# Kernel tuning notes

Measured on AMD Instinct MI355X. Metric: run time of the kernel, lower is better.

## Reference

```python
import jax, jax.numpy as jnp
import numpy as np

D = 3  # feature dim fixed by the module's Linear(3,3) layers
N = 6144

def _linear(x, w, b):
    # torch Linear: y = x @ W^T + b, W: [out,in]
    return x @ w.T + b

def setup_inputs() -> dict:
    key = jax.random.key(0)
    ks = jax.random.split(key, 20)
    lim = 1.0 / np.sqrt(D)  # torch default init bound
    def W(k):
        return jax.random.uniform(k, (D, D), jnp.float32, -lim, lim)
    def B(k):
        return jax.random.uniform(k, (D,), jnp.float32, -lim, lim)
    inp = {"x_data": jax.random.normal(ks[0], (N, D), jnp.float32)}
    names = ["q1", "q2", "q3", "q4", "k1", "k2", "v1", "v2", "b1b2"]
    for i, nm in enumerate(names):
        inp["w_" + nm] = W(ks[1 + 2 * i])
        inp["b_" + nm] = B(ks[2 + 2 * i])
    return inp

def reference(x_data, w_q1, b_q1, w_q2, b_q2, w_q3, b_q3, w_q4, b_q4,
              w_k1, b_k1, w_k2, b_k2, w_v1, b_v1, w_v2, b_v2, w_b1b2, b_b1b2):
    k1 = _linear(x_data, w_k1, b_k1)
    k2 = _linear(x_data, w_k2, b_k2)
    group1 = _linear(x_data, w_q1, b_q1) + _linear(x_data, w_q2, b_q2)
    group2 = _linear(x_data, w_q3, b_q3) + _linear(x_data, w_q4, b_q4)
    a1 = jax.nn.softmax(group1 @ k1.T, axis=1)  # [N, N]
    a2 = jax.nn.softmax(group2 @ k2.T, axis=1)  # [N, N]
    v1 = _linear(x_data, w_v1, b_v1)
    v2 = _linear(x_data, w_v2, b_v2)
    b = _linear(a1 @ v1 + a2 @ v2, w_b1b2, b_b1b2)  # [N, D]
    return (a1, b)
```

## Files before the change

kernel.cpp:

```cpp
#include <hip/hip_runtime.h>
#include <cstddef>

#define N_ROWS 6144
#define TR 8
#define NT 256
#define NBLK (N_ROWS / TR)

__device__ __forceinline__ float wredMax(float v) {
#pragma unroll
    for (int off = 32; off > 0; off >>= 1) v = fmaxf(v, __shfl_xor(v, off, 64));
    return v;
}
__device__ __forceinline__ float wredSum(float v) {
#pragma unroll
    for (int off = 32; off > 0; off >>= 1) v += __shfl_xor(v, off, 64);
    return v;
}

__global__ void proj_kernel(
    const float* __restrict__ x,
    const float* __restrict__ wq1, const float* __restrict__ bq1,
    const float* __restrict__ wq2, const float* __restrict__ bq2,
    const float* __restrict__ wq3, const float* __restrict__ bq3,
    const float* __restrict__ wq4, const float* __restrict__ bq4,
    const float* __restrict__ wk1, const float* __restrict__ bk1,
    const float* __restrict__ wk2, const float* __restrict__ bk2,
    const float* __restrict__ wv1, const float* __restrict__ bv1,
    const float* __restrict__ wv2, const float* __restrict__ bv2,
    float* __restrict__ gpack, float* __restrict__ kpack, float* __restrict__ vpack)
{
    int i = blockIdx.x * blockDim.x + threadIdx.x;
    if (i >= N_ROWS) return;
    float x0 = x[3*i+0], x1 = x[3*i+1], x2 = x[3*i+2];

    float g[8], k[8], v[8];
#pragma unroll
    for (int o = 0; o < 3; o++) {
        g[o]   = (wq1[3*o+0]+wq2[3*o+0])*x0 + (wq1[3*o+1]+wq2[3*o+1])*x1
               + (wq1[3*o+2]+wq2[3*o+2])*x2 + bq1[o] + bq2[o];
        g[3+o] = (wq3[3*o+0]+wq4[3*o+0])*x0 + (wq3[3*o+1]+wq4[3*o+1])*x1
               + (wq3[3*o+2]+wq4[3*o+2])*x2 + bq3[o] + bq4[o];
        k[o]   = wk1[3*o+0]*x0 + wk1[3*o+1]*x1 + wk1[3*o+2]*x2 + bk1[o];
        k[3+o] = wk2[3*o+0]*x0 + wk2[3*o+1]*x1 + wk2[3*o+2]*x2 + bk2[o];
        v[o]   = wv1[3*o+0]*x0 + wv1[3*o+1]*x1 + wv1[3*o+2]*x2 + bv1[o];
        v[3+o] = wv2[3*o+0]*x0 + wv2[3*o+1]*x1 + wv2[3*o+2]*x2 + bv2[o];
    }
    g[6]=g[7]=k[6]=k[7]=v[6]=v[7]=0.f;

    *(float4*)(gpack + (size_t)i*8)     = make_float4(g[0],g[1],g[2],g[3]);
    *(float4*)(gpack + (size_t)i*8 + 4) = make_float4(g[4],g[5],g[6],g[7]);
    *(float4*)(kpack + (size_t)i*8)     = make_float4(k[0],k[1],k[2],k[3]);
    *(float4*)(kpack + (size_t)i*8 + 4) = make_float4(k[4],k[5],k[6],k[7]);
    *(float4*)(vpack + (size_t)i*8)     = make_float4(v[0],v[1],v[2],v[3]);
    *(float4*)(vpack + (size_t)i*8 + 4) = make_float4(v[4],v[5],v[6],v[7]);
}

__global__ __launch_bounds__(NT) void attn_kernel(
    const float* __restrict__ gpack, const float* __restrict__ kpack,
    const float* __restrict__ vpack,
    const float* __restrict__ wb, const float* __restrict__ bb,
    float* __restrict__ out)
{
    const int row0 = blockIdx.x * TR;
    const int tid  = threadIdx.x;
    const int wave = tid >> 6;
    const int lane = tid & 63;

    __shared__ float red[4][3*TR];

    float g1x[TR], g1y[TR], g1z[TR], g2x[TR], g2y[TR], g2z[TR];
#pragma unroll
    for (int r = 0; r < TR; r++) {
        const float* gp = gpack + (size_t)(row0 + r) * 8;
        g1x[r]=gp[0]; g1y[r]=gp[1]; g1z[r]=gp[2];
        g2x[r]=gp[3]; g2y[r]=gp[4]; g2z[r]=gp[5];
    }

    float m1[TR], m2[TR];
#pragma unroll
    for (int r = 0; r < TR; r++) { m1[r] = -1e30f; m2[r] = -1e30f; }

    for (int j = tid; j < N_ROWS; j += NT) {
        const float4 ka = *(const float4*)(kpack + (size_t)j*8);
        const float2 kb = *(const float2*)(kpack + (size_t)j*8 + 4);
#pragma unroll
        for (int r = 0; r < TR; r++) {
            float s1 = g1x[r]*ka.x + g1y[r]*ka.y + g1z[r]*ka.z;
            float s2 = g2x[r]*ka.w + g2y[r]*kb.x + g2z[r]*kb.y;
            m1[r] = fmaxf(m1[r], s1);
            m2[r] = fmaxf(m2[r], s2);
        }
    }
#pragma unroll
    for (int r = 0; r < TR; r++) { m1[r] = wredMax(m1[r]); m2[r] = wredMax(m2[r]); }
    if (lane == 0) {
#pragma unroll
        for (int r = 0; r < TR; r++) { red[wave][r] = m1[r]; red[wave][TR+r] = m2[r]; }
    }
    __syncthreads();
#pragma unroll
    for (int r = 0; r < TR; r++) {
        m1[r] = fmaxf(fmaxf(red[0][r],    red[1][r]),    fmaxf(red[2][r],    red[3][r]));
        m2[r] = fmaxf(fmaxf(red[0][TR+r], red[1][TR+r]), fmaxf(red[2][TR+r], red[3][TR+r]));
    }
    __syncthreads();

    float l1[TR], l2[TR];
#pragma unroll
    for (int r = 0; r < TR; r++) { l1[r] = 0.f; l2[r] = 0.f; }

    for (int j = tid; j < N_ROWS; j += NT) {
        const float4 ka = *(const float4*)(kpack + (size_t)j*8);
        const float2 kb = *(const float2*)(kpack + (size_t)j*8 + 4);
#pragma unroll
        for (int r = 0; r < TR; r++) {
            float s1 = g1x[r]*ka.x + g1y[r]*ka.y + g1z[r]*ka.z;
            float s2 = g2x[r]*ka.w + g2y[r]*kb.x + g2z[r]*kb.y;
            l1[r] += __expf(s1 - m1[r]);
            l2[r] += __expf(s2 - m2[r]);
        }
    }
#pragma unroll
    for (int r = 0; r < TR; r++) { l1[r] = wredSum(l1[r]); l2[r] = wredSum(l2[r]); }
    if (lane == 0) {
#pragma unroll
        for (int r = 0; r < TR; r++) { red[wave][r] = l1[r]; red[wave][TR+r] = l2[r]; }
    }
    __syncthreads();
#pragma unroll
    for (int r = 0; r < TR; r++) {
        l1[r] = 1.0f / (red[0][r]    + red[1][r]    + red[2][r]    + red[3][r]);
        l2[r] = 1.0f / (red[0][TR+r] + red[1][TR+r] + red[2][TR+r] + red[3][TR+r]);
    }
    __syncthreads();

    float ox[TR], oy[TR], oz[TR];
#pragma unroll
    for (int r = 0; r < TR; r++) { ox[r]=0.f; oy[r]=0.f; oz[r]=0.f; }

    for (int j = tid; j < N_ROWS; j += NT) {
        const float4 ka = *(const float4*)(kpack + (size_t)j*8);
        const float2 kb = *(const float2*)(kpack + (size_t)j*8 + 4);
        const float4 va = *(const float4*)(vpack + (size_t)j*8);
        const float2 vb = *(const float2*)(vpack + (size_t)j*8 + 4);
#pragma unroll
        for (int r = 0; r < TR; r++) {
            float s1 = g1x[r]*ka.x + g1y[r]*ka.y + g1z[r]*ka.z;
            float s2 = g2x[r]*ka.w + g2y[r]*kb.x + g2z[r]*kb.y;
            float p1 = __expf(s1 - m1[r]) * l1[r];
            float p2 = __expf(s2 - m2[r]) * l2[r];
            out[(size_t)(row0 + r) * N_ROWS + j] = p1;
            ox[r] += p1*va.x + p2*va.w;
            oy[r] += p1*va.y + p2*vb.x;
            oz[r] += p1*va.z + p2*vb.y;
        }
    }
#pragma unroll
    for (int r = 0; r < TR; r++) { ox[r] = wredSum(ox[r]); oy[r] = wredSum(oy[r]); oz[r] = wredSum(oz[r]); }
    if (lane == 0) {
#pragma unroll
        for (int r = 0; r < TR; r++) {
            red[wave][r] = ox[r]; red[wave][TR+r] = oy[r]; red[wave][2*TR+r] = oz[r];
        }
    }
    __syncthreads();

    if (tid < TR) {
        float sox = red[0][tid]      + red[1][tid]      + red[2][tid]      + red[3][tid];
        float soy = red[0][TR+tid]   + red[1][TR+tid]   + red[2][TR+tid]   + red[3][TR+tid];
        float soz = red[0][2*TR+tid] + red[1][2*TR+tid] + red[2][2*TR+tid] + red[3][2*TR+tid];
        float b0 = wb[0]*sox + wb[1]*soy + wb[2]*soz + bb[0];
        float b1 = wb[3]*sox + wb[4]*soy + wb[5]*soz + bb[1];
        float b2 = wb[6]*sox + wb[7]*soy + wb[8]*soz + bb[2];
        size_t base = (size_t)N_ROWS * N_ROWS + (size_t)(row0 + tid) * 3;
        out[base+0] = b0; out[base+1] = b1; out[base+2] = b2;
    }
}

extern "C" void kernel_launch(void* const* d_in, const int* in_sizes, int n_in,
                              void* d_out, int out_size, void* d_ws, size_t ws_size,
                              hipStream_t stream) {
    const float* x   = (const float*)d_in[0];
    const float* wq1 = (const float*)d_in[1];  const float* bq1 = (const float*)d_in[2];
    const float* wq2 = (const float*)d_in[3];  const float* bq2 = (const float*)d_in[4];
    const float* wq3 = (const float*)d_in[5];  const float* bq3 = (const float*)d_in[6];
    const float* wq4 = (const float*)d_in[7];  const float* bq4 = (const float*)d_in[8];
    const float* wk1 = (const float*)d_in[9];  const float* bk1 = (const float*)d_in[10];
    const float* wk2 = (const float*)d_in[11]; const float* bk2 = (const float*)d_in[12];
    const float* wv1 = (const float*)d_in[13]; const float* bv1 = (const float*)d_in[14];
    const float* wv2 = (const float*)d_in[15]; const float* bv2 = (const float*)d_in[16];
    const float* wb  = (const float*)d_in[17]; const float* bb  = (const float*)d_in[18];

    float* ws    = (float*)d_ws;
    float* gpack = ws;
    float* kpack = ws + (size_t)N_ROWS * 8;
    float* vpack = ws + (size_t)N_ROWS * 16;
    float* out   = (float*)d_out;

    proj_kernel<<<N_ROWS / NT, NT, 0, stream>>>(
        x, wq1,bq1, wq2,bq2, wq3,bq3, wq4,bq4,
        wk1,bk1, wk2,bk2, wv1,bv1, wv2,bv2,
        gpack, kpack, vpack);

    attn_kernel<<<NBLK, NT, 0, stream>>>(gpack, kpack, vpack, wb, bb, out);
}
```

Before: 237.0 us.

## Replace per-row max pass with analytic bound and fuse sum with PV accumulation

Removes the exact row-max pass by computing a bound on each row's maximum score from per-dimension min/max of the keys, gathered in the projection kernel. The sum and value accumulation then run in one pass using unnormalised exp2, followed by a single pass that writes normalised probabilities with float4 stores. Keys and values move to a structure-of-arrays layout, and log2(e) is folded into the queries. This cuts three passes over keys to two and vectorises the output stores. The risk is that a loose max bound lets exp2 underflow for some rows.

```diff
diff --git a/kernel.cpp b/kernel.cpp
--- a/kernel.cpp
+++ b/kernel.cpp
@@ -5,6 +5,27 @@
 #define TR 8
 #define NT 256
 #define NBLK (N_ROWS / TR)
+#define PBLK (N_ROWS / NT)
+#define L2E 1.44269504088896340736f
+
+#if __has_builtin(__builtin_amdgcn_exp2f)
+#define EXP2F(x) __builtin_amdgcn_exp2f(x)
+#else
+#define EXP2F(x) exp2f(x)
+#endif
+#if __has_builtin(__builtin_amdgcn_logf)
+#define LOG2F(x) __builtin_amdgcn_logf(x)
+#else
+#define LOG2F(x) log2f(x)
+#endif
+
+#define WS_STATS (18 * N_ROWS)
+
+struct F4 { float v[4]; };
+__device__ __forceinline__ F4 ld4(const float* p) {
+    float4 t = *(const float4*)p;
+    F4 r; r.v[0]=t.x; r.v[1]=t.y; r.v[2]=t.z; r.v[3]=t.w; return r;
+}
 
 __device__ __forceinline__ float wredMax(float v) {
 #pragma unroll
@@ -17,7 +38,7 @@
     return v;
 }
 
-__global__ void proj_kernel(
+__global__ __launch_bounds__(NT) void proj_kernel(
     const float* __restrict__ x,
     const float* __restrict__ wq1, const float* __restrict__ bq1,
     const float* __restrict__ wq2, const float* __restrict__ bq2,
@@ -27,37 +48,60 @@
     const float* __restrict__ wk2, const float* __restrict__ bk2,
     const float* __restrict__ wv1, const float* __restrict__ bv1,
     const float* __restrict__ wv2, const float* __restrict__ bv2,
-    float* __restrict__ gpack, float* __restrict__ kpack, float* __restrict__ vpack)
+    float* __restrict__ ws)
 {
-    int i = blockIdx.x * blockDim.x + threadIdx.x;
-    if (i >= N_ROWS) return;
+    const int tid = threadIdx.x;
+    const int i = blockIdx.x * NT + tid;
+    const int wave = tid >> 6;
+    const int lane = tid & 63;
+
     float x0 = x[3*i+0], x1 = x[3*i+1], x2 = x[3*i+2];
 
-    float g[8], k[8], v[8];
+    float g1[3], g2[3], k1[3], k2[3], v1[3], v2[3];
 #pragma unroll
     for (int o = 0; o < 3; o++) {
-        g[o]   = (wq1[3*o+0]+wq2[3*o+0])*x0 + (wq1[3*o+1]+wq2[3*o+1])*x1
-               + (wq1[3*o+2]+wq2[3*o+2])*x2 + bq1[o] + bq2[o];
-        g[3+o] = (wq3[3*o+0]+wq4[3*o+0])*x0 + (wq3[3*o+1]+wq4[3*o+1])*x1
-               + (wq3[3*o+2]+wq4[3*o+2])*x2 + bq3[o] + bq4[o];
-        k[o]   = wk1[3*o+0]*x0 + wk1[3*o+1]*x1 + wk1[3*o+2]*x2 + bk1[o];
-        k[3+o] = wk2[3*o+0]*x0 + wk2[3*o+1]*x1 + wk2[3*o+2]*x2 + bk2[o];
-        v[o]   = wv1[3*o+0]*x0 + wv1[3*o+1]*x1 + wv1[3*o+2]*x2 + bv1[o];
-        v[3+o] = wv2[3*o+0]*x0 + wv2[3*o+1]*x1 + wv2[3*o+2]*x2 + bv2[o];
-    }
-    g[6]=g[7]=k[6]=k[7]=v[6]=v[7]=0.f;
-
-    *(float4*)(gpack + (size_t)i*8)     = make_float4(g[0],g[1],g[2],g[3]);
-    *(float4*)(gpack + (size_t)i*8 + 4) = make_float4(g[4],g[5],g[6],g[7]);
-    *(float4*)(kpack + (size_t)i*8)     = make_float4(k[0],k[1],k[2],k[3]);
-    *(float4*)(kpack + (size_t)i*8 + 4) = make_float4(k[4],k[5],k[6],k[7]);
-    *(float4*)(vpack + (size_t)i*8)     = make_float4(v[0],v[1],v[2],v[3]);
-    *(float4*)(vpack + (size_t)i*8 + 4) = make_float4(v[4],v[5],v[6],v[7]);
-}
-
-__global__ __launch_bounds__(NT) void attn_kernel(
-    const float* __restrict__ gpack, const float* __restrict__ kpack,
-    const float* __restrict__ vpack,
+        g1[o] = ((wq1[3*o+0]+wq2[3*o+0])*x0 + (wq1[3*o+1]+wq2[3*o+1])*x1
+              +  (wq1[3*o+2]+wq2[3*o+2])*x2 + bq1[o] + bq2[o]) * L2E;
+        g2[o] = ((wq3[3*o+0]+wq4[3*o+0])*x0 + (wq3[3*o+1]+wq4[3*o+1])*x1
+              +  (wq3[3*o+2]+wq4[3*o+2])*x2 + bq3[o] + bq4[o]) * L2E;
+        k1[o] = wk1[3*o+0]*x0 + wk1[3*o+1]*x1 + wk1[3*o+2]*x2 + bk1[o];
+        k2[o] = wk2[3*o+0]*x0 + wk2[3*o+1]*x1 + wk2[3*o+2]*x2 + bk2[o];
+        v1[o] = wv1[3*o+0]*x0 + wv1[3*o+1]*x1 + wv1[3*o+2]*x2 + bv1[o];
+        v2[o] = wv2[3*o+0]*x0 + wv2[3*o+1]*x1 + wv2[3*o+2]*x2 + bv2[o];
+    }
+
+#pragma unroll
+    for (int o = 0; o < 3; o++) {
+        ws[(0+o)*N_ROWS + i]  = g1[o];
+        ws[(3+o)*N_ROWS + i]  = g2[o];
+        ws[(6+o)*N_ROWS + i]  = k1[o];
+        ws[(9+o)*N_ROWS + i]  = k2[o];
+        ws[(12+o)*N_ROWS + i] = v1[o];
+        ws[(15+o)*N_ROWS + i] = v2[o];
+    }
+
+    float st[12] = { k1[0], k1[1], k1[2], -k1[0], -k1[1], -k1[2],
+                     k2[0], k2[1], k2[2], -k2[0], -k2[1], -k2[2] };
+    __shared__ float sred[4][12];
+#pragma unroll
+    for (int t = 0; t < 12; t++) st[t] = wredMax(st[t]);
+    if (lane == 0) {
+#pragma unroll
+        for (int t = 0; t < 12; t++) sred[wave][t] = st[t];
+    }
+    __syncthreads();
+    if (tid == 0) {
+#pragma unroll
+        for (int t = 0; t < 12; t++) {
+            float m = fmaxf(fmaxf(sred[0][t], sred[1][t]),
+                            fmaxf(sred[2][t], sred[3][t]));
+            ws[WS_STATS + blockIdx.x * 16 + t] = m;
+        }
+    }
+}
+
+__global__ __launch_bounds__(NT, 2) void attn_kernel(
+    const float* __restrict__ ws,
     const float* __restrict__ wb, const float* __restrict__ bb,
     float* __restrict__ out)
 {
@@ -66,113 +110,133 @@
     const int wave = tid >> 6;
     const int lane = tid & 63;
 
-    __shared__ float red[4][3*TR];
+    const float* k1x = ws + 6*N_ROWS;  const float* k1y = ws + 7*N_ROWS;
+    const float* k1z = ws + 8*N_ROWS;
+    const float* k2x = ws + 9*N_ROWS;  const float* k2y = ws + 10*N_ROWS;
+    const float* k2z = ws + 11*N_ROWS;
+    const float* v1x = ws + 12*N_ROWS; const float* v1y = ws + 13*N_ROWS;
+    const float* v1z = ws + 14*N_ROWS;
+    const float* v2x = ws + 15*N_ROWS; const float* v2y = ws + 16*N_ROWS;
+    const float* v2z = ws + 17*N_ROWS;
+
+    __shared__ float red[4][64];
+
+    float s12[12];
+#pragma unroll
+    for (int t = 0; t < 12; t++) s12[t] = -1e30f;
+    for (int b = 0; b < PBLK; b++) {
+        const float* sp = ws + WS_STATS + b * 16;
+#pragma unroll
+        for (int t = 0; t < 12; t++) s12[t] = fmaxf(s12[t], sp[t]);
+    }
 
     float g1x[TR], g1y[TR], g1z[TR], g2x[TR], g2y[TR], g2z[TR];
-#pragma unroll
-    for (int r = 0; r < TR; r++) {
-        const float* gp = gpack + (size_t)(row0 + r) * 8;
-        g1x[r]=gp[0]; g1y[r]=gp[1]; g1z[r]=gp[2];
-        g2x[r]=gp[3]; g2y[r]=gp[4]; g2z[r]=gp[5];
-    }
-
-    float m1[TR], m2[TR];
-#pragma unroll
-    for (int r = 0; r < TR; r++) { m1[r] = -1e30f; m2[r] = -1e30f; }
-
-    for (int j = tid; j < N_ROWS; j += NT) {
-        const float4 ka = *(const float4*)(kpack + (size_t)j*8);
-        const float2 kb = *(const float2*)(kpack + (size_t)j*8 + 4);
+    float c1[TR], c2[TR];
+#pragma unroll
+    for (int r = 0; r < TR; r++) {
+        int i = row0 + r;
+        g1x[r] = ws[0*N_ROWS+i]; g1y[r] = ws[1*N_ROWS+i]; g1z[r] = ws[2*N_ROWS+i];
+        g2x[r] = ws[3*N_ROWS+i]; g2y[r] = ws[4*N_ROWS+i]; g2z[r] = ws[5*N_ROWS+i];
+        float m1 = fmaxf(g1x[r]*s12[0], g1x[r]*-s12[3])
+                 + fmaxf(g1y[r]*s12[1], g1y[r]*-s12[4])
+                 + fmaxf(g1z[r]*s12[2], g1z[r]*-s12[5]);
+        float m2 = fmaxf(g2x[r]*s12[6], g2x[r]*-s12[9])
+                 + fmaxf(g2y[r]*s12[7], g2y[r]*-s12[10])
+                 + fmaxf(g2z[r]*s12[8], g2z[r]*-s12[11]);
+        c1[r] = -m1;
+        c2[r] = -m2;
+    }
+
+    float l1[TR], l2[TR];
+    float o1x[TR], o1y[TR], o1z[TR], o2x[TR], o2y[TR], o2z[TR];
+#pragma unroll
+    for (int r = 0; r < TR; r++) {
+        l1[r]=0.f; l2[r]=0.f;
+        o1x[r]=0.f; o1y[r]=0.f; o1z[r]=0.f;
+        o2x[r]=0.f; o2y[r]=0.f; o2z[r]=0.f;
+    }
+
+    for (int it = 0; it < N_ROWS / (NT*4); it++) {
+        const int j0 = it*(NT*4) + tid*4;
+        F4 KX1 = ld4(k1x+j0), KY1 = ld4(k1y+j0), KZ1 = ld4(k1z+j0);
+        F4 KX2 = ld4(k2x+j0), KY2 = ld4(k2y+j0), KZ2 = ld4(k2z+j0);
+        F4 VX1 = ld4(v1x+j0), VY1 = ld4(v1y+j0), VZ1 = ld4(v1z+j0);
+        F4 VX2 = ld4(v2x+j0), VY2 = ld4(v2y+j0), VZ2 = ld4(v2z+j0);
 #pragma unroll
         for (int r = 0; r < TR; r++) {
-            float s1 = g1x[r]*ka.x + g1y[r]*ka.y + g1z[r]*ka.z;
-            float s2 = g2x[r]*ka.w + g2y[r]*kb.x + g2z[r]*kb.y;
-            m1[r] = fmaxf(m1[r], s1);
-            m2[r] = fmaxf(m2[r], s2);
-        }
-    }
-#pragma unroll
-    for (int r = 0; r < TR; r++) { m1[r] = wredMax(m1[r]); m2[r] = wredMax(m2[r]); }
-    if (lane == 0) {
-#pragma unroll
-        for (int r = 0; r < TR; r++) { red[wave][r] = m1[r]; red[wave][TR+r] = m2[r]; }
+#pragma unroll
+            for (int jj = 0; jj < 4; jj++) {
+                float t1 = fmaf(g1z[r], KZ1.v[jj],
+                            fmaf(g1y[r], KY1.v[jj],
+                             fmaf(g1x[r], KX1.v[jj], c1[r])));
+                float t2 = fmaf(g2z[r], KZ2.v[jj],
+                            fmaf(g2y[r], KY2.v[jj],
+                             fmaf(g2x[r], KX2.v[jj], c2[r])));
+                float e1 = EXP2F(t1);
+                float e2 = EXP2F(t2);
+                l1[r] += e1; l2[r] += e2;
+                o1x[r] = fmaf(e1, VX1.v[jj], o1x[r]);
+                o1y[r] = fmaf(e1, VY1.v[jj], o1y[r]);
+                o1z[r] = fmaf(e1, VZ1.v[jj], o1z[r]);
+                o2x[r] = fmaf(e2, VX2.v[jj], o2x[r]);
+                o2y[r] = fmaf(e2, VY2.v[jj], o2y[r]);
+                o2z[r] = fmaf(e2, VZ2.v[jj], o2z[r]);
+            }
+        }
+    }
+
+#pragma unroll
+    for (int r = 0; r < TR; r++) {
+        l1[r]  = wredSum(l1[r]);  l2[r]  = wredSum(l2[r]);
+        o1x[r] = wredSum(o1x[r]); o1y[r] = wredSum(o1y[r]); o1z[r] = wredSum(o1z[r]);
+        o2x[r] = wredSum(o2x[r]); o2y[r] = wredSum(o2y[r]); o2z[r] = wredSum(o2z[r]);
+        if (lane == 0) {
+            red[wave][r*8+0]=l1[r];  red[wave][r*8+1]=l2[r];
+            red[wave][r*8+2]=o1x[r]; red[wave][r*8+3]=o1y[r]; red[wave][r*8+4]=o1z[r];
+            red[wave][r*8+5]=o2x[r]; red[wave][r*8+6]=o2y[r]; red[wave][r*8+7]=o2z[r];
+        }
     }
     __syncthreads();
-#pragma unroll
-    for (int r = 0; r < TR; r++) {
-        m1[r] = fmaxf(fmaxf(red[0][r],    red[1][r]),    fmaxf(red[2][r],    red[3][r]));
-        m2[r] = fmaxf(fmaxf(red[0][TR+r], red[1][TR+r]), fmaxf(red[2][TR+r], red[3][TR+r]));
-    }
-    __syncthreads();
-
-    float l1[TR], l2[TR];
-#pragma unroll
-    for (int r = 0; r < TR; r++) { l1[r] = 0.f; l2[r] = 0.f; }
-
-    for (int j = tid; j < N_ROWS; j += NT) {
-        const float4 ka = *(const float4*)(kpack + (size_t)j*8);
-        const float2 kb = *(const float2*)(kpack + (size_t)j*8 + 4);
+
+    float c1p[TR];
+#pragma unroll
+    for (int r = 0; r < TR; r++) {
+        float l1t = red[0][r*8] + red[1][r*8] + red[2][r*8] + red[3][r*8];
+        c1p[r] = c1[r] - LOG2F(l1t);
+    }
+
+    for (int it = 0; it < N_ROWS / (NT*4); it++) {
+        const int j0 = it*(NT*4) + tid*4;
+        F4 KX = ld4(k1x+j0), KY = ld4(k1y+j0), KZ = ld4(k1z+j0);
 #pragma unroll
         for (int r = 0; r < TR; r++) {
-            float s1 = g1x[r]*ka.x + g1y[r]*ka.y + g1z[r]*ka.z;
-            float s2 = g2x[r]*ka.w + g2y[r]*kb.x + g2z[r]*kb.y;
-            l1[r] += __expf(s1 - m1[r]);
-            l2[r] += __expf(s2 - m2[r]);
-        }
-    }
-#pragma unroll
-    for (int r = 0; r < TR; r++) { l1[r] = wredSum(l1[r]); l2[r] = wredSum(l2[r]); }
-    if (lane == 0) {
-#pragma unroll
-        for (int r = 0; r < TR; r++) { red[wave][r] = l1[r]; red[wave][TR+r] = l2[r]; }
-    }
-    __syncthreads();
-#pragma unroll
-    for (int r = 0; r < TR; r++) {
-        l1[r] = 1.0f / (red[0][r]    + red[1][r]    + red[2][r]    + red[3][r]);
-        l2[r] = 1.0f / (red[0][TR+r] + red[1][TR+r] + red[2][TR+r] + red[3][TR+r]);
-    }
-    __syncthreads();
-
-    float ox[TR], oy[TR], oz[TR];
-#pragma unroll
-    for (int r = 0; r < TR; r++) { ox[r]=0.f; oy[r]=0.f; oz[r]=0.f; }
-
-    for (int j = tid; j < N_ROWS; j += NT) {
-        const float4 ka = *(const float4*)(kpack + (size_t)j*8);
-        const float2 kb = *(const float2*)(kpack + (size_t)j*8 + 4);
-        const float4 va = *(const float4*)(vpack + (size_t)j*8);
-        const float2 vb = *(const float2*)(vpack + (size_t)j*8 + 4);
-#pragma unroll
-        for (int r = 0; r < TR; r++) {
-            float s1 = g1x[r]*ka.x + g1y[r]*ka.y + g1z[r]*ka.z;
-            float s2 = g2x[r]*ka.w + g2y[r]*kb.x + g2z[r]*kb.y;
-            float p1 = __expf(s1 - m1[r]) * l1[r];
-            float p2 = __expf(s2 - m2[r]) * l2[r];
-            out[(size_t)(row0 + r) * N_ROWS + j] = p1;
-            ox[r] += p1*va.x + p2*va.w;
-            oy[r] += p1*va.y + p2*vb.x;
-            oz[r] += p1*va.z + p2*vb.y;
-        }
-    }
-#pragma unroll
-    for (int r = 0; r < TR; r++) { ox[r] = wredSum(ox[r]); oy[r] = wredSum(oy[r]); oz[r] = wredSum(oz[r]); }
-    if (lane == 0) {
-#pragma unroll
-        for (int r = 0; r < TR; r++) {
-            red[wave][r] = ox[r]; red[wave][TR+r] = oy[r]; red[wave][2*TR+r] = oz[r];
-        }
-    }
-    __syncthreads();
+            float4 pv;
+            pv.x = EXP2F(fmaf(g1z[r], KZ.v[0], fmaf(g1y[r], KY.v[0], fmaf(g1x[r], KX.v[0], c1p[r]))));
+            pv.y = EXP2F(fmaf(g1z[r], KZ.v[1], fmaf(g1y[r], KY.v[1], fmaf(g1x[r], KX.v[1], c1p[r]))));
+            pv.z = EXP2F(fmaf(g1z[r], KZ.v[2], fmaf(g1y[r], KY.v[2], fmaf(g1x[r], KX.v[2], c1p[r]))));
+            pv.w = EXP2F(fmaf(g1z[r], KZ.v[3], fmaf(g1y[r], KY.v[3], fmaf(g1x[r], KX.v[3], c1p[r]))));
+            *(float4*)(out + (size_t)(row0 + r) * N_ROWS + j0) = pv;
+        }
+    }
 
     if (tid < TR) {
-        float sox = red[0][tid]      + red[1][tid]      + red[2][tid]      + red[3][tid];
-        float soy = red[0][TR+tid]   + red[1][TR+tid]   + red[2][TR+tid]   + red[3][TR+tid];
-        float soz = red[0][2*TR+tid] + red[1][2*TR+tid] + red[2][2*TR+tid] + red[3][2*TR+tid];
-        float b0 = wb[0]*sox + wb[1]*soy + wb[2]*soz + bb[0];
-        float b1 = wb[3]*sox + wb[4]*soy + wb[5]*soz + bb[1];
-        float b2 = wb[6]*sox + wb[7]*soy + wb[8]*soz + bb[2];
-        size_t base = (size_t)N_ROWS * N_ROWS + (size_t)(row0 + tid) * 3;
+        int r = tid;
+        float l1t = red[0][r*8+0]+red[1][r*8+0]+red[2][r*8+0]+red[3][r*8+0];
+        float l2t = red[0][r*8+1]+red[1][r*8+1]+red[2][r*8+1]+red[3][r*8+1];
+        float sx1 = red[0][r*8+2]+red[1][r*8+2]+red[2][r*8+2]+red[3][r*8+2];
+        float sy1 = red[0][r*8+3]+red[1][r*8+3]+red[2][r*8+3]+red[3][r*8+3];
+        float sz1 = red[0][r*8+4]+red[1][r*8+4]+red[2][r*8+4]+red[3][r*8+4];
+        float sx2 = red[0][r*8+5]+red[1][r*8+5]+red[2][r*8+5]+red[3][r*8+5];
+        float sy2 = red[0][r*8+6]+red[1][r*8+6]+red[2][r*8+6]+red[3][r*8+6];
+        float sz2 = red[0][r*8+7]+red[1][r*8+7]+red[2][r*8+7]+red[3][r*8+7];
+        float r1 = 1.0f / l1t, r2 = 1.0f / l2t;
+        float ox = sx1*r1 + sx2*r2;
+        float oy = sy1*r1 + sy2*r2;
+        float oz = sz1*r1 + sz2*r2;
+        float b0 = wb[0]*ox + wb[1]*oy + wb[2]*oz + bb[0];
+        float b1 = wb[3]*ox + wb[4]*oy + wb[5]*oz + bb[1];
+        float b2 = wb[6]*ox + wb[7]*oy + wb[8]*oz + bb[2];
+        size_t base = (size_t)N_ROWS * N_ROWS + (size_t)(row0 + r) * 3;
         out[base+0] = b0; out[base+1] = b1; out[base+2] = b2;
     }
 }
@@ -191,16 +255,12 @@
     const float* wv2 = (const float*)d_in[15]; const float* bv2 = (const float*)d_in[16];
     const float* wb  = (const float*)d_in[17]; const float* bb  = (const float*)d_in[18];
 
-    float* ws    = (float*)d_ws;
-    float* gpack = ws;
-    float* kpack = ws + (size_t)N_ROWS * 8;
-    float* vpack = ws + (size_t)N_ROWS * 16;
-    float* out   = (float*)d_out;
-
-    proj_kernel<<<N_ROWS / NT, NT, 0, stream>>>(
+    float* ws  = (float*)d_ws;
+    float* out = (float*)d_out;
+
+    proj_kernel<<<PBLK, NT, 0, stream>>>(
         x, wq1,bq1, wq2,bq2, wq3,bq3, wq4,bq4,
-        wk1,bk1, wk2,bk2, wv1,bv1, wv2,bv2,
-        gpack, kpack, vpack);
-
-    attn_kernel<<<NBLK, NT, 0, stream>>>(gpack, kpack, vpack, wb, bb, out);
-}
+        wk1,bk1, wk2,bk2, wv1,bv1, wv2,bv2, ws);
+
+    attn_kernel<<<NBLK, NT, 0, stream>>>(ws, wb, bb, out);
+}
```

After: 221.5 us. -6.6%, faster.
